# Kernel optimization log

Measured on AMD Instinct MI355X. Metric: run time of the kernel, lower is better.

## Reference

```python
import jax, jax.numpy as jnp
import numpy as np

B, L, D, H = 4, 2048, 256, 512


def silu_backward(x):
    s = jax.nn.silu(x)
    return s + jax.nn.sigmoid(x) * (1.0 - s)


def setup_inputs() -> dict:
    key = jax.random.key(0)
    ks = jax.random.split(key, 12)
    sc = 0.02
    return {
        "x": jax.random.normal(ks[0], (B, L, D), jnp.float32),
        "W1": jax.random.normal(ks[1], (B, H, D), jnp.float32) * sc,
        "W2": jax.random.normal(ks[2], (B, D, H), jnp.float32) * sc,
        "Wq": jax.random.normal(ks[3], (D, D), jnp.float32) * sc,
        "bq": jnp.zeros((D,), jnp.float32),
        "Wk": jax.random.normal(ks[4], (D, D), jnp.float32) * sc,
        "bk": jnp.zeros((D,), jnp.float32),
        "Wv": jax.random.normal(ks[5], (D, D), jnp.float32) * sc,
        "bv": jnp.zeros((D,), jnp.float32),
        "w_lr": jax.random.normal(ks[6], (D,), jnp.float32) * sc,
        "b_lr": jnp.zeros((), jnp.float32),
        "w_wd": jax.random.normal(ks[7], (D,), jnp.float32) * sc,
        "b_wd": jnp.zeros((), jnp.float32),
        "log_base_lr": jnp.asarray(np.log(0.1), jnp.float32),
        "log_base_wd": jnp.asarray(np.log(0.5), jnp.float32),
    }


def reference(x, W1, W2, Wq, bq, Wk, bk, Wv, bv, w_lr, b_lr, w_wd, b_wd, log_base_lr, log_base_wd):
    b, l, d = x.shape
    query = x @ Wq + bq
    key = x @ Wk + bk
    value = x @ Wv + bv
    lr = jnp.exp(log_base_lr) * jax.nn.sigmoid(x @ w_lr + b_lr)          # [b,l]
    log_wd = jnp.log(1.0 - jnp.exp(log_base_wd) * jax.nn.sigmoid(x @ w_wd + b_wd))  # [b,l]

    wd_cross = jnp.exp(jnp.cumsum(log_wd, axis=1))                       # [b,l]
    idx = jnp.arange(l)
    strict_upper = idx[:, None] < idx[None, :]                           # (m, j): j > m
    A = jnp.where(strict_upper[None], log_wd[:, None, :], 0.0)           # [b,m,j]
    wd_inner = jnp.exp(jnp.cumsum(A, axis=2)) * (idx[:, None] <= idx[None, :])[None]  # [b,m,j]

    X1 = key
    Z1 = jnp.einsum('bhd,bld->blh', W1, X1)
    X2 = jax.nn.silu(Z1)
    Z2 = jnp.einsum('bdh,blh->bld', W2, X2)
    grad_Z2 = Z2 - value
    grad_X2 = jnp.einsum('bdh,bld->blh', W2, grad_Z2)
    grad_Z1 = silu_backward(Z1) * grad_X2

    X1_ = query
    mask_X1X1_ = jnp.einsum('bld,bmd->blm', X1, X1_) * wd_inner
    Z1_inner = -jnp.einsum('blh,bl,blm->bmh', grad_Z1, lr, mask_X1X1_)
    Z1_cross = jnp.einsum('bhd,bld,bl->blh', W1, X1_, wd_cross)
    Z1_ = Z1_inner + Z1_cross

    W1_next = (-jnp.einsum('blh,bl,bld->bhd', grad_Z1, lr * wd_inner[:, :, -1], X1)
               + W1 * wd_cross[:, -1][:, None, None])

    X2_ = jax.nn.silu(Z1_)
    mask_X2X2_ = jnp.einsum('blh,bmh->blm', X2, X2_) * wd_inner
    Z2_inner = -jnp.einsum('bld,bl,blm->bmd', grad_Z2, lr, mask_X2X2_)
    Z2_cross = jnp.einsum('bdh,blh,bl->bld', W2, X2_, wd_cross)
    Z2_ = Z2_inner + Z2_cross

    W2_next = (-jnp.einsum('bld,bl,blh->bdh', grad_Z2, lr * wd_inner[:, :, -1], X2)
               + W2 * wd_cross[:, -1][:, None, None])

    return (Z2_, W1_next, W2_next)
```

## Files before the change

### kernel.cpp

```cpp
#include <hip/hip_runtime.h>

typedef __bf16 bf16;
typedef __bf16 bf16x8 __attribute__((ext_vector_type(8)));
typedef __bf16 bf16x4 __attribute__((ext_vector_type(4)));
typedef float  f32x4  __attribute__((ext_vector_type(4)));

#define SB 72
#define CUTOFF -18.0

__device__ __forceinline__ float silu_f(float x){
  float s = 1.f/(1.f+__expf(-x));
  return x*s;
}
__device__ __forceinline__ float silu_bwd_f(float x){
  float s = 1.f/(1.f+__expf(-x));
  float si = x*s;
  return si + s*(1.f-si);
}

struct MArgs {
  const bf16* A; const bf16* B;
  long sA, sB;
  int lda, ldb;
  int M, N, K;
  int mode;
  float* Cf; long sCf;
  bf16*  Cb; long sCb;
  bf16*  Cb2; long sCb2;
  bf16*  Ct;  long sCt;  int ldct;
  int ldc;
  const float* auxf; int ldax; long sAuxf;
  const bf16*  auxb; long sAuxb;
  const float* rowv; long sRowv;
  const double* cd;  long sCd;
  const float* ks;   long sKs;
  const float* clp;  long sClp;
  bf16* Q; bf16* Ko; float* Vo; const float* bqkv;
};

template<int TM>
__device__ __forceinline__ void gemm_body(const MArgs& g, int bm, int bn, int bz)
{
  const int row0 = bm*TM, col0 = bn*64;
  constexpr int NI  = TM/32;
  constexpr int TPR = 256/TM;
  constexpr int EPR = 64/TPR;
  constexpr int NCH = EPR/8;

  const bf16* A = g.A + (long)bz*g.sA;
  const bf16* B = g.B + (long)bz*g.sB;
  const float* ksp = g.ks ? g.ks + (long)bz*g.sKs : (const float*)0;
  const double* cd = g.cd ? g.cd + (long)bz*g.sCd : (const double*)0;
  float* Cf = g.Cf ? g.Cf + (long)bz*g.sCf : (float*)0;
  bf16* Cb  = g.Cb ? g.Cb + (long)bz*g.sCb : (bf16*)0;
  bf16* Cb2 = g.Cb2 ? g.Cb2 + (long)bz*g.sCb2 : (bf16*)0;
  bf16* Ct  = g.Ct ? g.Ct + (long)bz*g.sCt : (bf16*)0;
  const float* auxf = g.auxf ? g.auxf + (long)bz*g.sAuxf : (const float*)0;
  const bf16*  auxb = g.auxb ? g.auxb + (long)bz*g.sAuxb : (const bf16*)0;
  const float* rowv = g.rowv ? g.rowv + (long)bz*g.sRowv : (const float*)0;

  const int tid = threadIdx.x;
  const int mode = g.mode;
  const int lane = tid & 63;
  const int w = tid >> 6;
  const int wr = (w >> 1) * (TM/2), wc = (w & 1) * 32;
  const int l15 = lane & 15;
  const int quad = lane >> 4;

  __shared__ __align__(16) bf16 As[TM*SB];
  __shared__ __align__(16) bf16 Bs[64*SB];

  f32x4 acc[NI][2];
  #pragma unroll
  for (int i=0;i<NI;i++)
    #pragma unroll
    for (int j=0;j<2;j++)
      #pragma unroll
      for (int r=0;r<4;r++) acc[i][j][r] = 0.f;

  const int rowA = tid / TPR, kA = (tid % TPR) * EPR;
  const int rowB = tid >> 2,  kB = (tid & 3) * 16;

  int klo = 0;
  if (cd && ksp) {
    const double cref = cd[g.K-1];
    while (klo + 64 < g.K && (cref - cd[klo+63]) < CUTOFF) klo += 64;
  }

  for (int k0 = klo; k0 < g.K; k0 += 64) {
    {
      const bf16* s = A + (long)(row0+rowA)*g.lda + k0 + kA;
      bf16x8 v[NCH];
      #pragma unroll
      for (int p=0;p<NCH;p++) v[p] = *(const bf16x8*)(s + p*8);
      if (ksp) {
        #pragma unroll
        for (int p=0;p<NCH;p++)
          #pragma unroll
          for (int i=0;i<8;i++)
            v[p][i] = (bf16)((float)v[p][i] * ksp[k0+kA+p*8+i]);
      }
      #pragma unroll
      for (int p=0;p<NCH;p++) *(bf16x8*)&As[rowA*SB + kA + p*8] = v[p];
    }
    {
      const bf16* s = B + (long)(col0+rowB)*g.ldb + k0 + kB;
      *(bf16x8*)&Bs[rowB*SB + kB]     = *(const bf16x8*)s;
      *(bf16x8*)&Bs[rowB*SB + kB + 8] = *(const bf16x8*)(s+8);
    }
    __syncthreads();
    #pragma unroll
    for (int ch=0; ch<2; ch++){
      bf16x8 af[NI], bf2[2];
      #pragma unroll
      for (int i=0;i<NI;i++) af[i]  = *(const bf16x8*)&As[(wr + i*16 + l15)*SB + ch*32 + quad*8];
      #pragma unroll
      for (int j=0;j<2;j++) bf2[j] = *(const bf16x8*)&Bs[(wc + j*16 + l15)*SB + ch*32 + quad*8];
      #pragma unroll
      for (int i=0;i<NI;i++)
        #pragma unroll
        for (int j=0;j<2;j++)
          acc[i][j] = __builtin_amdgcn_mfma_f32_16x16x32_bf16(af[i], bf2[j], acc[i][j], 0, 0, 0);
    }
    __syncthreads();
  }

  float clv = 0.f;
  if (mode == 10) clv = *(g.clp + (long)bz*g.sClp);

  #pragma unroll
  for (int i=0;i<NI;i++){
    const int rb = row0 + wr + i*16 + quad*4;
    #pragma unroll
    for (int j=0;j<2;j++){
      const int c = col0 + wc + j*16 + l15;
      bf16 tv[4]; bool doT = false;
      #pragma unroll
      for (int reg=0; reg<4; reg++){
        const int r = rb + reg;
        float v = acc[i][j][reg];
        const long co = (long)r*g.ldc + c;
        switch (mode) {
          case 1: {
            Cb[co]  = (bf16)v;
            bf16 sv = (bf16)silu_f(v);
            Cb2[co] = sv;
            tv[reg] = sv; doT = true;
          } break;
          case 2: {
            bf16 o = (bf16)(v - auxf[(long)r*g.ldax + c]);
            Cb[co] = o; tv[reg] = o; doT = true;
          } break;
          case 3: {
            bf16 o = (bf16)(silu_bwd_f((float)auxb[(long)r*g.ldax + c]) * v * rowv[r]);
            Cb[co] = o; tv[reg] = o; doT = true;
          } break;
          case 10: {
            Cf[co] = v + auxf[(long)r*g.ldax + c]*clv;
          } break;
          case 11: {
            float o = v + g.bqkv[c];
            if (c < 256)      g.Q [(long)r*256 + c]       = (bf16)o;
            else if (c < 512) { g.Ko[(long)r*256 + (c-256)] = (bf16)o; tv[reg] = (bf16)o; doT = true; }
            else              g.Vo[(long)r*256 + (c-512)] = o;
          } break;
        }
      }
      if (doT && Ct) {
        bf16x4 t4 = { tv[0], tv[1], tv[2], tv[3] };
        if (mode == 11) {
          const int b = rb / g.ldct, l = rb % g.ldct;
          *(bf16x4*)&Ct[(long)b*g.sCt + (long)(c-256)*g.ldct + l] = t4;
        } else {
          *(bf16x4*)&Ct[(long)c*g.ldct + rb] = t4;
        }
      }
    }
  }
}

__global__ __launch_bounds__(256)
void mfma_gemm128(MArgs g){ gemm_body<128>(g, blockIdx.x, blockIdx.y, blockIdx.z); }

__global__ __launch_bounds__(256)
void mfma_gemm64(MArgs g){ gemm_body<64>(g, blockIdx.x, blockIdx.y, blockIdx.z); }

__global__ __launch_bounds__(256)
void wnext_gemm(MArgs g1, MArgs g2){
  const int z = blockIdx.z;
  const MArgs& g = (z < 4) ? g1 : g2;
  const int bz = z & 3;
  if ((int)blockIdx.x*128 >= g.M || (int)blockIdx.y*64 >= g.N) return;
  gemm_body<128>(g, blockIdx.x, blockIdx.y, bz);
}

struct PArgs {
  const bf16 *A, *B1;
  long sA, sB1;
  const double* cd; long sCd;
  const float* lrv; long sLr;
  bf16* P;
};

template<int KS64, int ISLR>
__global__ __launch_bounds__(256)
void pgen(PArgs g)
{
  const int mt = blockIdx.x, slot = blockIdx.y, bz = blockIdx.z;
  const int m0 = mt*64;
  const int l0 = (m0 & ~127) - slot*128;
  if (l0 < 0) return;
  const double* cd = g.cd + (long)bz*g.sCd;
  const int lref = (l0+127 < m0) ? (l0+127) : m0;
  if (cd[m0] - cd[lref] < CUTOFF) return;

  const int K1 = KS64*64;
  const bf16* A  = g.A  + (long)bz*g.sA;
  const bf16* B1 = g.B1 + (long)bz*g.sB1;
  const float* lrv = ISLR ? (g.lrv + (long)bz*g.sLr) : (const float*)0;

  const int tid = threadIdx.x;
  const int lane = tid & 63, w = tid >> 6;
  const int wr = (w>>1)*32, wc = (w&1)*64;
  const int l15 = lane & 15, quad = lane >> 4;
  const int rowA = tid >> 2, kA = (tid & 3) * 16;
  const int rowB = tid >> 1, kB = (tid & 1) * 32;

  __shared__ __align__(16) bf16 As[64*SB];
  __shared__ __align__(16) bf16 Bs[128*SB];

  f32x4 O[2][4];
  #pragma unroll
  for (int i=0;i<2;i++)
    #pragma unroll
    for (int j=0;j<4;j++)
      #pragma unroll
      for (int r=0;r<4;r++) O[i][j][r] = 0.f;

  for (int ks=0; ks<KS64; ks++){
    const int k0 = ks*64;
    {
      const bf16* s = A + (long)(m0+rowA)*K1 + k0 + kA;
      *(bf16x8*)&As[rowA*SB + kA]     = *(const bf16x8*)s;
      *(bf16x8*)&As[rowA*SB + kA + 8] = *(const bf16x8*)(s+8);
    }
    {
      const bf16* s = B1 + (long)(l0+rowB)*K1 + k0 + kB;
      #pragma unroll
      for (int p=0;p<4;p++) *(bf16x8*)&Bs[rowB*SB + kB + p*8] = *(const bf16x8*)(s + p*8);
    }
    __syncthreads();
    #pragma unroll
    for (int ch=0; ch<2; ch++){
      bf16x8 af[2], bfr[4];
      #pragma unroll
      for (int i=0;i<2;i++) af[i]  = *(const bf16x8*)&As[(wr + i*16 + l15)*SB + ch*32 + quad*8];
      #pragma unroll
      for (int j=0;j<4;j++) bfr[j] = *(const bf16x8*)&Bs[(wc + j*16 + l15)*SB + ch*32 + quad*8];
      #pragma unroll
      for (int i=0;i<2;i++)
        #pragma unroll
        for (int j=0;j<4;j++)
          O[i][j] = __builtin_amdgcn_mfma_f32_16x16x32_bf16(af[i], bfr[j], O[i][j], 0, 0, 0);
    }
    __syncthreads();
  }

  bf16* Pt = g.P + (((long)bz*32 + mt)*3 + slot) * (64*128);
  float cl[4], lv[4];
  #pragma unroll
  for (int j=0;j<4;j++){
    const int l = l0 + wc + j*16 + l15;
    cl[j] = (float)cd[l];
    if (ISLR) lv[j] = lrv[l];
  }
  #pragma unroll
  for (int i=0;i<2;i++)
    #pragma unroll
    for (int reg=0; reg<4; reg++){
      const int mloc = wr + i*16 + quad*4 + reg;
      const int m = m0 + mloc;
      const float cm = (float)cd[m];
      #pragma unroll
      for (int j=0;j<4;j++){
        const int lloc = wc + j*16 + l15;
        const int l = l0 + lloc;
        float v = -O[i][j][reg] * __expf(cm - cl[j]);
        if (ISLR) v *= lv[j];
        if (l > m) v = 0.f;
        Pt[mloc*128 + lloc] = (bf16)v;
      }
    }
}

struct CArgs {
  const bf16 *A, *W, *P, *B2;
  long sA, sW, sB2;
  int ldb2;
  const double* cd; long sCd;
  const float* wdc; long sWdc;
  float* Cf; long sCf;
  bf16* Cb; long sCb;
  int ldc;
};

template<int KS64, int SILU, int ZSPLIT>
__global__ __launch_bounds__(256)
void cons(CArgs g)
{
  const int mt = blockIdx.x;
  const int m0 = mt*64, n0 = blockIdx.y*64;
  const int bz   = ZSPLIT ? (blockIdx.z >> 1) : blockIdx.z;
  const int half = ZSPLIT ? (blockIdx.z & 1)  : 0;
  const int K1 = KS64*64;
  const bf16* A  = g.A  + (long)bz*g.sA;
  const bf16* W  = g.W  + (long)bz*g.sW;
  const bf16* B2 = g.B2 + (long)bz*g.sB2;
  const double* cd = g.cd + (long)bz*g.sCd;
  const float* wdc = g.wdc + (long)bz*g.sWdc;

  const int tid = threadIdx.x;
  const int lane = tid & 63, w = tid >> 6;
  const int wr = (w>>1)*32, wc = (w&1)*32;
  const int l15 = lane & 15, quad = lane >> 4;
  const int rowA = tid >> 2, kA = (tid & 3) * 16;

  bool alive[3];
  int nalive = 0;
  #pragma unroll
  for (int s=0;s<3;s++){
    const int l0 = (m0 & ~127) - s*128;
    bool a = (l0 >= 0);
    if (a) {
      const int lref = (l0+127 < m0) ? (l0+127) : m0;
      a = (cd[m0] - cd[lref] >= CUTOFF);
    }
    alive[s] = a; nalive += a ? 1 : 0;
  }
  if (ZSPLIT && half == 1 && nalive == 0) return;

  __shared__ __align__(16) bf16 As[64*SB];
  __shared__ __align__(16) bf16 Bs[64*SB];

  f32x4 O[2][2];
  #pragma unroll
  for (int i=0;i<2;i++)
    #pragma unroll
    for (int j=0;j<2;j++)
      #pragma unroll
      for (int r=0;r<4;r++) O[i][j][r] = 0.f;

  if (half == 0) {
    for (int ks=0; ks<KS64; ks++){
      const int k0 = ks*64;
      {
        const bf16* s = A + (long)(m0+rowA)*K1 + k0 + kA;
        *(bf16x8*)&As[rowA*SB + kA]     = *(const bf16x8*)s;
        *(bf16x8*)&As[rowA*SB + kA + 8] = *(const bf16x8*)(s+8);
      }
      {
        const bf16* s = W + (long)(n0+rowA)*K1 + k0 + kA;
        *(bf16x8*)&Bs[rowA*SB + kA]     = *(const bf16x8*)s;
        *(bf16x8*)&Bs[rowA*SB + kA + 8] = *(const bf16x8*)(s+8);
      }
      __syncthreads();
      #pragma unroll
      for (int ch=0; ch<2; ch++){
        bf16x8 af[2], bfr[2];
        #pragma unroll
        for (int i=0;i<2;i++) af[i]  = *(const bf16x8*)&As[(wr + i*16 + l15)*SB + ch*32 + quad*8];
        #pragma unroll
        for (int j=0;j<2;j++) bfr[j] = *(const bf16x8*)&Bs[(wc + j*16 + l15)*SB + ch*32 + quad*8];
        #pragma unroll
        for (int i=0;i<2;i++)
          #pragma unroll
          for (int j=0;j<2;j++)
            O[i][j] = __builtin_amdgcn_mfma_f32_16x16x32_bf16(af[i], bfr[j], O[i][j], 0, 0, 0);
      }
      __syncthreads();
    }
    #pragma unroll
    for (int i=0;i<2;i++)
      #pragma unroll
      for (int reg=0; reg<4; reg++){
        const float s = wdc[m0 + wr + i*16 + quad*4 + reg];
        #pragma unroll
        for (int j=0;j<2;j++) O[i][j][reg] *= s;
      }
  }

  if (!ZSPLIT || half == 1) {
    for (int s=0; s<3; s++){
      if (!alive[s]) continue;
      const int l0 = (m0 & ~127) - s*128;
      const bf16* Pt = g.P + (((long)bz*32 + mt)*3 + s) * (64*128);
      for (int hk=0; hk<2; hk++){
        {
          const bf16* sp = Pt + (long)rowA*128 + hk*64 + kA;
          *(bf16x8*)&As[rowA*SB + kA]     = *(const bf16x8*)sp;
          *(bf16x8*)&As[rowA*SB + kA + 8] = *(const bf16x8*)(sp+8);
        }
        {
          const bf16* sp = B2 + (long)(n0+rowA)*g.ldb2 + l0 + hk*64 + kA;
          *(bf16x8*)&Bs[rowA*SB + kA]     = *(const bf16x8*)sp;
          *(bf16x8*)&Bs[rowA*SB + kA + 8] = *(const bf16x8*)(sp+8);
        }
        __syncthreads();
        #pragma unroll
        for (int ch=0; ch<2; ch++){
          bf16x8 af[2], bfr[2];
          #pragma unroll
          for (int i=0;i<2;i++) af[i]  = *(const bf16x8*)&As[(wr + i*16 + l15)*SB + ch*32 + quad*8];
          #pragma unroll
          for (int j=0;j<2;j++) bfr[j] = *(const bf16x8*)&Bs[(wc + j*16 + l15)*SB + ch*32 + quad*8];
          #pragma unroll
          for (int i=0;i<2;i++)
            #pragma unroll
            for (int j=0;j<2;j++)
              O[i][j] = __builtin_amdgcn_mfma_f32_16x16x32_bf16(af[i], bfr[j], O[i][j], 0, 0, 0);
        }
        __syncthreads();
      }
    }
  }

  #pragma unroll
  for (int i=0;i<2;i++){
    const int rb = m0 + wr + i*16 + quad*4;
    #pragma unroll
    for (int j=0;j<2;j++){
      const int c = n0 + wc + j*16 + l15;
      #pragma unroll
      for (int reg=0; reg<4; reg++){
        const long co = (long)(rb+reg)*g.ldc + c;
        if (ZSPLIT)     unsafeAtomicAdd(&g.Cf[(long)bz*g.sCf + co], O[i][j][reg]);
        else if (SILU)  g.Cb[(long)bz*g.sCb + co] = (bf16)silu_f(O[i][j][reg]);
        else            g.Cf[(long)bz*g.sCf + co] = O[i][j][reg];
      }
    }
  }
}

struct FrontArgs {
  const float *x, *W1, *W2, *Wq, *Wk, *Wv;
  bf16 *xb, *W1b, *W2b, *Wqkvt, *W2t;
  float* out0;
  const float *wlr, *blr, *wwd, *bwd, *lbl, *lbw;
  float *lr, *lw;
  long LD4, HD4, HD;
};

__global__ __launch_bounds__(256)
void front_kernel(FrontArgs f)
{
  __shared__ bf16 t[64][72];
  const int bid = blockIdx.x;
  const int tid = threadIdx.x;

  if (bid < 1536) {
    const float* src; bf16* dst; long n; long base;
    if (bid < 1024)      { src = f.x;  dst = f.xb;  n = f.LD4; base = (long)bid*2048; }
    else if (bid < 1280) { src = f.W1; dst = f.W1b; n = f.HD4; base = (long)(bid-1024)*2048; }
    else                 { src = f.W2; dst = f.W2b; n = f.HD4; base = (long)(bid-1280)*2048; }
    long i = base + (long)tid*8;
    if (i >= n) return;
    float4 a = *(const float4*)&src[i];
    float4 b = *(const float4*)&src[i+4];
    bf16x8 o;
    o[0]=(bf16)a.x; o[1]=(bf16)a.y; o[2]=(bf16)a.z; o[3]=(bf16)a.w;
    o[4]=(bf16)b.x; o[5]=(bf16)b.y; o[6]=(bf16)b.z; o[7]=(bf16)b.w;
    *(bf16x8*)&dst[i] = o;
    return;
  }
  if (bid < 2560) {
    long i = (long)(bid-1536)*2048 + (long)tid*8;
    float4 z = {0.f,0.f,0.f,0.f};
    *(float4*)&f.out0[i]   = z;
    *(float4*)&f.out0[i+4] = z;
    return;
  }
  if (bid < 2736) {
    const float* ip; bf16* op; int R, C; int r0, c0;
    if (bid < 2608) {
      const int r = bid - 2560;
      const int z = r >> 4, rem = r & 15;
      ip = z==0 ? f.Wq : (z==1 ? f.Wk : f.Wv);
      op = f.Wqkvt + (long)z*256*256;
      R = 256; C = 256;
      r0 = (rem & 3)*64; c0 = (rem >> 2)*64;
    } else {
      const int r = bid - 2608;
      const int b = r >> 5, rem = r & 31;
      ip = f.W2 + (long)b*f.HD;
      op = f.W2t + (long)b*f.HD;
      R = 256; C = 512;
      r0 = (rem & 3)*64; c0 = (rem >> 2)*64;
    }
    const int lr_ = tid>>2, lc = (tid&3)*16;
    #pragma unroll
    for (int q=0;q<4;q++){
      float4 a = *(const float4*)&ip[(long)(r0+lr_)*C + c0+lc + q*4];
      t[lr_][lc+q*4+0] = (bf16)a.x; t[lr_][lc+q*4+1] = (bf16)a.y;
      t[lr_][lc+q*4+2] = (bf16)a.z; t[lr_][lc+q*4+3] = (bf16)a.w;
    }
    __syncthreads();
    const int oc = tid>>2, orr = (tid&3)*16;
    bf16x8 u, v;
    #pragma unroll
    for (int i=0;i<8;i++){ u[i] = t[orr+i][oc]; v[i] = t[orr+8+i][oc]; }
    *(bf16x8*)&op[(long)(c0+oc)*R + r0+orr]   = u;
    *(bf16x8*)&op[(long)(c0+oc)*R + r0+orr+8] = v;
    return;
  }
  {
    const int row  = (bid-2736)*4 + (tid >> 6);
    const int lane = tid & 63;
    const float4 a = ((const float4*)(f.x + (long)row*256))[lane];
    const float4 u = ((const float4*)f.wlr)[lane];
    const float4 w = ((const float4*)f.wwd)[lane];
    float d1 = a.x*u.x + a.y*u.y + a.z*u.z + a.w*u.w;
    float d2 = a.x*w.x + a.y*w.y + a.z*w.z + a.w*w.w;
    #pragma unroll
    for (int off=32; off; off>>=1) {
      d1 += __shfl_down(d1, off);
      d2 += __shfl_down(d2, off);
    }
    if (lane == 0) {
      float s1 = 1.f/(1.f+expf(-(d1 + f.blr[0])));
      f.lr[row] = expf(f.lbl[0]) * s1;
      float s2 = 1.f/(1.f+expf(-(d2 + f.bwd[0])));
      f.lw[row] = logf(1.f - expf(f.lbw[0]) * s2);
    }
  }
}

__global__ __launch_bounds__(256)
void cumsum_kernel(const float* __restrict__ lw, const float* __restrict__ lr,
                   double* __restrict__ cd, float* __restrict__ wdc,
                   float* __restrict__ se1, float* __restrict__ se2, int L,
                   const float* __restrict__ bq, const float* __restrict__ bk,
                   const float* __restrict__ bv, float* __restrict__ bqkv)
{
  const int b = blockIdx.x;
  const int t = threadIdx.x;
  if (b == 4) {
    for (int i = t; i < 768; i += 256)
      bqkv[i] = (i<256) ? bq[i] : ((i<512) ? bk[i-256] : bv[i-512]);
    return;
  }
  const float* lwb = lw + (long)b*L;
  __shared__ double sum_s[256];
  double loc[8];
  double s = 0.0;
  #pragma unroll
  for (int i=0;i<8;i++){ s += (double)lwb[t*8+i]; loc[i] = s; }
  sum_s[t] = s;
  __syncthreads();
  for (int off=1; off<256; off<<=1){
    double v = 0.0;
    if (t >= off) v = sum_s[t-off];
    __syncthreads();
    sum_s[t] += v;
    __syncthreads();
  }
  const double prefix = (t > 0) ? sum_s[t-1] : 0.0;
  const double total  = sum_s[255];
  #pragma unroll
  for (int i=0;i<8;i++){
    double c = prefix + loc[i];
    long idx = (long)b*L + t*8 + i;
    cd[idx]  = c;
    wdc[idx] = (float)exp(c);
    double e = exp(total - c);
    se1[idx] = (float)(-e);
    se2[idx] = (float)(-e) * lr[idx];
  }
}

extern "C" void kernel_launch(void* const* d_in, const int* in_sizes, int n_in,
                              void* d_out, int out_size, void* d_ws, size_t ws_size,
                              hipStream_t stream)
{
  const int Bn = 4, L = 2048, D = 256, H = 512;
  const long LD = (long)L*D, LH = (long)L*H, HD = (long)H*D;

  const float* x   = (const float*)d_in[0];
  const float* W1  = (const float*)d_in[1];
  const float* W2  = (const float*)d_in[2];
  const float* Wq  = (const float*)d_in[3];
  const float* bq  = (const float*)d_in[4];
  const float* Wk  = (const float*)d_in[5];
  const float* bk  = (const float*)d_in[6];
  const float* Wv  = (const float*)d_in[7];
  const float* bv  = (const float*)d_in[8];
  const float* wlr = (const float*)d_in[9];
  const float* blr = (const float*)d_in[10];
  const float* wwd = (const float*)d_in[11];
  const float* bwd = (const float*)d_in[12];
  const float* lbl = (const float*)d_in[13];
  const float* lbw = (const float*)d_in[14];
  (void)in_sizes; (void)n_in; (void)out_size; (void)ws_size;

  float* out0 = (float*)d_out;
  float* out1 = out0 + (long)Bn*LD;
  float* out2 = out1 + (long)Bn*HD;

  char* wsp = (char*)d_ws;
  size_t off = 0;
  auto alloc = [&](size_t bytes)->void*{
    void* p = wsp + off; off += (bytes + 255) & ~(size_t)255; return p;
  };
  bf16* xb    = (bf16*)alloc((size_t)Bn*LD*2);
  bf16* Wqkvt = (bf16*)alloc((size_t)3*D*D*2);
  float* bqkv = (float*)alloc((size_t)3*D*4);
  bf16* W1b  = (bf16*)alloc((size_t)Bn*HD*2);
  bf16* W2b  = (bf16*)alloc((size_t)Bn*HD*2);
  bf16* W2t  = (bf16*)alloc((size_t)Bn*HD*2);
  bf16* Qb   = (bf16*)alloc((size_t)Bn*LD*2);
  bf16* Kb   = (bf16*)alloc((size_t)Bn*LD*2);
  bf16* Kt   = (bf16*)alloc((size_t)Bn*LD*2);
  float* Vf  = (float*)alloc((size_t)Bn*LD*4);
  bf16* Z1b  = (bf16*)alloc((size_t)Bn*LH*2);
  bf16* X2b  = (bf16*)alloc((size_t)Bn*LH*2);
  bf16* X2t  = (bf16*)alloc((size_t)Bn*LH*2);
  bf16* gZb  = (bf16*)alloc((size_t)Bn*LD*2);
  bf16* gZt  = (bf16*)alloc((size_t)Bn*LD*2);
  bf16* A1b  = (bf16*)alloc((size_t)Bn*LH*2);
  bf16* A1t  = (bf16*)alloc((size_t)Bn*LH*2);
  bf16* X2_b = (bf16*)alloc((size_t)Bn*LH*2);
  bf16* Pb1  = (bf16*)alloc((size_t)Bn*32*3*64*128*2);
  bf16* Pb2  = (bf16*)alloc((size_t)Bn*32*3*64*128*2);
  float* lrb = (float*)alloc((size_t)Bn*L*4);
  float* lwb = (float*)alloc((size_t)Bn*L*4);
  float* wdc = (float*)alloc((size_t)Bn*L*4);
  float* se1 = (float*)alloc((size_t)Bn*L*4);
  float* se2 = (float*)alloc((size_t)Bn*L*4);
  double* cdb = (double*)alloc((size_t)Bn*L*8);

  auto run128 = [&](const MArgs& g, int Z){
    dim3 grid(g.M/128, g.N/64, Z);
    mfma_gemm128<<<grid, 256, 0, stream>>>(g);
  };
  auto run64 = [&](const MArgs& g, int Z){
    dim3 grid(g.M/64, g.N/64, Z);
    mfma_gemm64<<<grid, 256, 0, stream>>>(g);
  };

  {
    FrontArgs f{};
    f.x = x; f.W1 = W1; f.W2 = W2; f.Wq = Wq; f.Wk = Wk; f.Wv = Wv;
    f.xb = xb; f.W1b = W1b; f.W2b = W2b; f.Wqkvt = Wqkvt; f.W2t = W2t;
    f.out0 = out0;
    f.wlr = wlr; f.blr = blr; f.wwd = wwd; f.bwd = bwd; f.lbl = lbl; f.lbw = lbw;
    f.lr = lrb; f.lw = lwb;
    f.LD4 = Bn*LD; f.HD4 = Bn*HD; f.HD = HD;
    front_kernel<<<dim3(4784), 256, 0, stream>>>(f);
  }
  cumsum_kernel<<<dim3(5), 256, 0, stream>>>(lwb, lrb, cdb, wdc, se1, se2, L, bq, bk, bv, bqkv);

  {
    MArgs g{}; g.A = xb; g.lda = D; g.B = Wqkvt; g.ldb = D;
    g.M = Bn*L; g.N = 3*D; g.K = D; g.mode = 11; g.ldc = 0;
    g.Q = Qb; g.Ko = Kb; g.Vo = Vf; g.bqkv = bqkv;
    g.Ct = Kt; g.sCt = LD; g.ldct = L;
    run128(g, 1);
  }
  {
    MArgs g{}; g.A = Kb; g.lda = D; g.sA = LD; g.B = W1b; g.ldb = D; g.sB = HD;
    g.M = L; g.N = H; g.K = D; g.mode = 1; g.ldc = H;
    g.Cb = Z1b; g.sCb = LH; g.Cb2 = X2b; g.sCb2 = LH;
    g.Ct = X2t; g.sCt = LH; g.ldct = L; run64(g, Bn);
  }
  {
    MArgs g{}; g.A = X2b; g.lda = H; g.sA = LH; g.B = W2b; g.ldb = H; g.sB = HD;
    g.M = L; g.N = D; g.K = H; g.mode = 2; g.ldc = D;
    g.auxf = Vf; g.ldax = D; g.sAuxf = LD; g.Cb = gZb; g.sCb = LD;
    g.Ct = gZt; g.sCt = LD; g.ldct = L; run64(g, Bn);
  }
  {
    MArgs g{}; g.A = gZb; g.lda = D; g.sA = LD; g.B = W2t; g.ldb = D; g.sB = HD;
    g.M = L; g.N = H; g.K = D; g.mode = 3; g.ldc = H;
    g.auxb = Z1b; g.ldax = H; g.sAuxb = LH; g.rowv = lrb; g.sRowv = L;
    g.Cb = A1b; g.sCb = LH;
    g.Ct = A1t; g.sCt = LH; g.ldct = L; run64(g, Bn);
  }
  {
    PArgs p{};
    p.A = Qb; p.sA = LD; p.B1 = Kb; p.sB1 = LD;
    p.cd = cdb; p.sCd = L; p.P = Pb1;
    pgen<4,0><<<dim3(32,3,Bn), 256, 0, stream>>>(p);
  }
  {
    CArgs c{};
    c.A = Qb; c.sA = LD; c.W = W1b; c.sW = HD;
    c.P = Pb1; c.B2 = A1t; c.sB2 = LH; c.ldb2 = L;
    c.cd = cdb; c.sCd = L; c.wdc = wdc; c.sWdc = L;
    c.Cb = X2_b; c.sCb = LH; c.ldc = H;
    cons<4,1,0><<<dim3(32, H/64, Bn), 256, 0, stream>>>(c);
  }
  {
    PArgs p{};
    p.A = X2_b; p.sA = LH; p.B1 = X2b; p.sB1 = LH;
    p.cd = cdb; p.sCd = L; p.lrv = lrb; p.sLr = L; p.P = Pb2;
    pgen<8,1><<<dim3(32,3,Bn), 256, 0, stream>>>(p);
  }
  {
    CArgs c{};
    c.A = X2_b; c.sA = LH; c.W = W2b; c.sW = HD;
    c.P = Pb2; c.B2 = gZt; c.sB2 = LD; c.ldb2 = L;
    c.cd = cdb; c.sCd = L; c.wdc = wdc; c.sWdc = L;
    c.Cf = out0; c.sCf = LD; c.ldc = D;
    cons<8,0,1><<<dim3(32, D/64, Bn*2), 256, 0, stream>>>(c);
  }
  {
    MArgs g1{}; g1.A = A1t; g1.lda = L; g1.sA = LH; g1.B = Kt; g1.ldb = L; g1.sB = LD;
    g1.M = H; g1.N = D; g1.K = L; g1.mode = 10; g1.ldc = D;
    g1.ks = se1; g1.sKs = L; g1.cd = cdb; g1.sCd = L;
    g1.auxf = W1; g1.ldax = D; g1.sAuxf = HD; g1.clp = wdc + (L-1); g1.sClp = L;
    g1.Cf = out1; g1.sCf = HD;

    MArgs g2{}; g2.A = gZt; g2.lda = L; g2.sA = LD; g2.B = X2t; g2.ldb = L; g2.sB = LH;
    g2.M = D; g2.N = H; g2.K = L; g2.mode = 10; g2.ldc = H;
    g2.ks = se2; g2.sKs = L; g2.cd = cdb; g2.sCd = L;
    g2.auxf = W2; g2.ldax = H; g2.sAuxf = HD; g2.clp = wdc + (L-1); g2.sClp = L;
    g2.Cf = out2; g2.sCf = HD;

    wnext_gemm<<<dim3(4,8,8), 256, 0, stream>>>(g1, g2);
  }
}
```

Baseline: 235.3 us.

## Stage transposed GEMM epilogue stores through LDS and fold K-scaling into producers

Transposed outputs (X2t, gZt, A1t, Kt) are now first written into the shared-memory tile and then stored to global memory as coalesced 16-byte rows, instead of scattered 4-element column writes. The per-k scale factors that the W_next GEMM applied while loading its A operand are moved into the producer epilogues: X2t is pre-scaled by se2, and a second scaled copy A1s is written in mode 3. The unused row-major A1b output is dropped. This removes the conversion-heavy inner-loop scaling from the long-K GEMM and improves store coalescing. The cost is an extra transposed buffer, a sync in the epilogue, and slightly different bf16 rounding order.

```diff
diff --git a/kernel.cpp b/kernel.cpp
--- a/kernel.cpp
+++ b/kernel.cpp
@@ -28,12 +28,13 @@
   bf16*  Cb; long sCb;
   bf16*  Cb2; long sCb2;
   bf16*  Ct;  long sCt;  int ldct;
+  bf16*  Ct2; long sCt2;
   int ldc;
   const float* auxf; int ldax; long sAuxf;
   const bf16*  auxb; long sAuxb;
   const float* rowv; long sRowv;
+  const float* rowv2; long sRowv2;
   const double* cd;  long sCd;
-  const float* ks;   long sKs;
   const float* clp;  long sClp;
   bf16* Q; bf16* Ko; float* Vo; const float* bqkv;
 };
@@ -41,6 +42,11 @@
 template<int TM>
 __device__ __forceinline__ void gemm_body(const MArgs& g, int bm, int bn, int bz)
 {
+  constexpr int TTP = (TM==64) ? 72 : 136;
+  __shared__ __align__(16) bf16 sh[(TM+64)*SB];
+  bf16* As = sh;
+  bf16* Bs = sh + TM*SB;
+
   const int row0 = bm*TM, col0 = bn*64;
   constexpr int NI  = TM/32;
   constexpr int TPR = 256/TM;
@@ -49,15 +55,16 @@
 
   const bf16* A = g.A + (long)bz*g.sA;
   const bf16* B = g.B + (long)bz*g.sB;
-  const float* ksp = g.ks ? g.ks + (long)bz*g.sKs : (const float*)0;
   const double* cd = g.cd ? g.cd + (long)bz*g.sCd : (const double*)0;
   float* Cf = g.Cf ? g.Cf + (long)bz*g.sCf : (float*)0;
   bf16* Cb  = g.Cb ? g.Cb + (long)bz*g.sCb : (bf16*)0;
   bf16* Cb2 = g.Cb2 ? g.Cb2 + (long)bz*g.sCb2 : (bf16*)0;
   bf16* Ct  = g.Ct ? g.Ct + (long)bz*g.sCt : (bf16*)0;
+  bf16* Ct2 = g.Ct2 ? g.Ct2 + (long)bz*g.sCt2 : (bf16*)0;
   const float* auxf = g.auxf ? g.auxf + (long)bz*g.sAuxf : (const float*)0;
   const bf16*  auxb = g.auxb ? g.auxb + (long)bz*g.sAuxb : (const bf16*)0;
   const float* rowv = g.rowv ? g.rowv + (long)bz*g.sRowv : (const float*)0;
+  const float* rowv2 = g.rowv2 ? g.rowv2 + (long)bz*g.sRowv2 : (const float*)0;
 
   const int tid = threadIdx.x;
   const int mode = g.mode;
@@ -67,9 +74,6 @@
   const int l15 = lane & 15;
   const int quad = lane >> 4;
 
-  __shared__ __align__(16) bf16 As[TM*SB];
-  __shared__ __align__(16) bf16 Bs[64*SB];
-
   f32x4 acc[NI][2];
   #pragma unroll
   for (int i=0;i<NI;i++)
@@ -82,7 +86,7 @@
   const int rowB = tid >> 2,  kB = (tid & 3) * 16;
 
   int klo = 0;
-  if (cd && ksp) {
+  if (cd) {
     const double cref = cd[g.K-1];
     while (klo + 64 < g.K && (cref - cd[klo+63]) < CUTOFF) klo += 64;
   }
@@ -90,18 +94,9 @@
   for (int k0 = klo; k0 < g.K; k0 += 64) {
     {
       const bf16* s = A + (long)(row0+rowA)*g.lda + k0 + kA;
-      bf16x8 v[NCH];
-      #pragma unroll
-      for (int p=0;p<NCH;p++) v[p] = *(const bf16x8*)(s + p*8);
-      if (ksp) {
-        #pragma unroll
-        for (int p=0;p<NCH;p++)
-          #pragma unroll
-          for (int i=0;i<8;i++)
-            v[p][i] = (bf16)((float)v[p][i] * ksp[k0+kA+p*8+i]);
-      }
-      #pragma unroll
-      for (int p=0;p<NCH;p++) *(bf16x8*)&As[rowA*SB + kA + p*8] = v[p];
+      #pragma unroll
+      for (int p=0;p<NCH;p++)
+        *(bf16x8*)&As[rowA*SB + kA + p*8] = *(const bf16x8*)(s + p*8);
     }
     {
       const bf16* s = B + (long)(col0+rowB)*g.ldb + k0 + kB;
@@ -128,13 +123,18 @@
   float clv = 0.f;
   if (mode == 10) clv = *(g.clp + (long)bz*g.sClp);
 
+  const bool hasT = (TM==64) ? (mode==1 || mode==2 || mode==3)
+                             : (mode==11 && col0 >= 256 && col0 < 512);
+
   #pragma unroll
   for (int i=0;i<NI;i++){
     const int rb = row0 + wr + i*16 + quad*4;
+    const int rloc = wr + i*16 + quad*4;
     #pragma unroll
     for (int j=0;j<2;j++){
       const int c = col0 + wc + j*16 + l15;
-      bf16 tv[4]; bool doT = false;
+      const int cloc = wc + j*16 + l15;
+      bf16 tv[4], tv2[4]; bool doT = false, doT2 = false;
       #pragma unroll
       for (int reg=0; reg<4; reg++){
         const int r = rb + reg;
@@ -143,17 +143,19 @@
         switch (mode) {
           case 1: {
             Cb[co]  = (bf16)v;
-            bf16 sv = (bf16)silu_f(v);
-            Cb2[co] = sv;
-            tv[reg] = sv; doT = true;
+            float sv = silu_f(v);
+            Cb2[co] = (bf16)sv;
+            tv[reg] = (bf16)(sv * rowv[r]); doT = true;
           } break;
           case 2: {
             bf16 o = (bf16)(v - auxf[(long)r*g.ldax + c]);
             Cb[co] = o; tv[reg] = o; doT = true;
           } break;
           case 3: {
-            bf16 o = (bf16)(silu_bwd_f((float)auxb[(long)r*g.ldax + c]) * v * rowv[r]);
-            Cb[co] = o; tv[reg] = o; doT = true;
+            float v3 = silu_bwd_f((float)auxb[(long)r*g.ldax + c]) * v * rowv[r];
+            tv[reg]  = (bf16)v3;
+            tv2[reg] = (bf16)(v3 * rowv2[r]);
+            doT = true; doT2 = true;
           } break;
           case 10: {
             Cf[co] = v + auxf[(long)r*g.ldax + c]*clv;
@@ -166,15 +168,40 @@
           } break;
         }
       }
-      if (doT && Ct) {
+      if (hasT && doT) {
         bf16x4 t4 = { tv[0], tv[1], tv[2], tv[3] };
-        if (mode == 11) {
-          const int b = rb / g.ldct, l = rb % g.ldct;
-          *(bf16x4*)&Ct[(long)b*g.sCt + (long)(c-256)*g.ldct + l] = t4;
-        } else {
-          *(bf16x4*)&Ct[(long)c*g.ldct + rb] = t4;
+        *(bf16x4*)&sh[cloc*TTP + rloc] = t4;
+        if (doT2) {
+          bf16x4 t4b = { tv2[0], tv2[1], tv2[2], tv2[3] };
+          *(bf16x4*)&sh[64*72 + cloc*TTP + rloc] = t4b;
         }
       }
+    }
+  }
+
+  if (hasT) {
+    __syncthreads();
+    if constexpr (TM == 64) {
+      const int cl = tid >> 2, rl = (tid & 3)*16;
+      bf16x8 u0 = *(const bf16x8*)&sh[cl*72 + rl];
+      bf16x8 u1 = *(const bf16x8*)&sh[cl*72 + rl + 8];
+      bf16* d = Ct + (long)(col0+cl)*g.ldct + row0 + rl;
+      *(bf16x8*)d       = u0;
+      *(bf16x8*)(d + 8) = u1;
+      if (mode == 3) {
+        bf16x8 v0 = *(const bf16x8*)&sh[64*72 + cl*72 + rl];
+        bf16x8 v1 = *(const bf16x8*)&sh[64*72 + cl*72 + rl + 8];
+        bf16* d2 = Ct2 + (long)(col0+cl)*g.ldct + row0 + rl;
+        *(bf16x8*)d2       = v0;
+        *(bf16x8*)(d2 + 8) = v1;
+      }
+    } else {
+      const int cl = tid >> 2, rl = (tid & 3)*32;
+      const int b = row0 / g.ldct, l0r = row0 % g.ldct;
+      bf16* d = Ct + (long)b*g.sCt + (long)(col0-256+cl)*g.ldct + l0r + rl;
+      #pragma unroll
+      for (int p=0;p<4;p++)
+        *(bf16x8*)(d + p*8) = *(const bf16x8*)&sh[cl*136 + rl + p*8];
     }
   }
 }
@@ -625,8 +652,8 @@
   bf16* X2t  = (bf16*)alloc((size_t)Bn*LH*2);
   bf16* gZb  = (bf16*)alloc((size_t)Bn*LD*2);
   bf16* gZt  = (bf16*)alloc((size_t)Bn*LD*2);
-  bf16* A1b  = (bf16*)alloc((size_t)Bn*LH*2);
   bf16* A1t  = (bf16*)alloc((size_t)Bn*LH*2);
+  bf16* A1s  = (bf16*)alloc((size_t)Bn*LH*2);
   bf16* X2_b = (bf16*)alloc((size_t)Bn*LH*2);
   bf16* Pb1  = (bf16*)alloc((size_t)Bn*32*3*64*128*2);
   bf16* Pb2  = (bf16*)alloc((size_t)Bn*32*3*64*128*2);
@@ -669,7 +696,9 @@
     MArgs g{}; g.A = Kb; g.lda = D; g.sA = LD; g.B = W1b; g.ldb = D; g.sB = HD;
     g.M = L; g.N = H; g.K = D; g.mode = 1; g.ldc = H;
     g.Cb = Z1b; g.sCb = LH; g.Cb2 = X2b; g.sCb2 = LH;
-    g.Ct = X2t; g.sCt = LH; g.ldct = L; run64(g, Bn);
+    g.Ct = X2t; g.sCt = LH; g.ldct = L;
+    g.rowv = se2; g.sRowv = L;
+    run64(g, Bn);
   }
   {
     MArgs g{}; g.A = X2b; g.lda = H; g.sA = LH; g.B = W2b; g.ldb = H; g.sB = HD;
@@ -680,9 +709,11 @@
   {
     MArgs g{}; g.A = gZb; g.lda = D; g.sA = LD; g.B = W2t; g.ldb = D; g.sB = HD;
     g.M = L; g.N = H; g.K = D; g.mode = 3; g.ldc = H;
-    g.auxb = Z1b; g.ldax = H; g.sAuxb = LH; g.rowv = lrb; g.sRowv = L;
-    g.Cb = A1b; g.sCb = LH;
-    g.Ct = A1t; g.sCt = LH; g.ldct = L; run64(g, Bn);
+    g.auxb = Z1b; g.ldax = H; g.sAuxb = LH;
+    g.rowv = lrb; g.sRowv = L; g.rowv2 = se1; g.sRowv2 = L;
+    g.Ct = A1t; g.sCt = LH; g.ldct = L;
+    g.Ct2 = A1s; g.sCt2 = LH;
+    run64(g, Bn);
   }
   {
     PArgs p{};
@@ -713,15 +744,15 @@
     cons<8,0,1><<<dim3(32, D/64, Bn*2), 256, 0, stream>>>(c);
   }
   {
-    MArgs g1{}; g1.A = A1t; g1.lda = L; g1.sA = LH; g1.B = Kt; g1.ldb = L; g1.sB = LD;
+    MArgs g1{}; g1.A = A1s; g1.lda = L; g1.sA = LH; g1.B = Kt; g1.ldb = L; g1.sB = LD;
     g1.M = H; g1.N = D; g1.K = L; g1.mode = 10; g1.ldc = D;
-    g1.ks = se1; g1.sKs = L; g1.cd = cdb; g1.sCd = L;
+    g1.cd = cdb; g1.sCd = L;
     g1.auxf = W1; g1.ldax = D; g1.sAuxf = HD; g1.clp = wdc + (L-1); g1.sClp = L;
     g1.Cf = out1; g1.sCf = HD;
 
     MArgs g2{}; g2.A = gZt; g2.lda = L; g2.sA = LD; g2.B = X2t; g2.ldb = L; g2.sB = LH;
     g2.M = D; g2.N = H; g2.K = L; g2.mode = 10; g2.ldc = H;
-    g2.ks = se2; g2.sKs = L; g2.cd = cdb; g2.sCd = L;
+    g2.cd = cdb; g2.sCd = L;
     g2.auxf = W2; g2.ldax = H; g2.sAuxf = HD; g2.clp = wdc + (L-1); g2.sClp = L;
     g2.Cf = out2; g2.sCf = HD;
 
```

Result: no change. 232.3 us (-1.3%).
